# Kernel optimization log

Measured on AMD Instinct MI355X. Metric: run time of the kernel, lower is better.

The kernel has to match this reference:

```python
import jax, jax.numpy as jnp
import numpy as np

B, N, C, D = 4, 8192, 256, 256
WS = [2048, 4096, 8192]
RS = [1, 2, 4]
HEAD_IDX = 0


def setup_inputs() -> dict:
    key = jax.random.key(0)
    k1, k2, k3, k4 = jax.random.split(key, 4)
    scale = 1.0 / np.sqrt(C).astype(np.float32)
    x = jax.random.normal(k1, (B, N, C), jnp.float32)
    Wq = jax.random.normal(k2, (C, D), jnp.float32) * scale
    Wk = jax.random.normal(k3, (C, D), jnp.float32) * scale
    Wv = jax.random.normal(k4, (C, D), jnp.float32) * scale
    return {"x": x, "Wq": Wq, "Wk": Wk, "Wv": Wv}


def _causal_attn(v, Wq, Wk, Wv):
    # v: [Bseg, m, c] -> out [Bseg, m, D], denom [Bseg, m] (= sum_k exp(score))
    q = v @ Wq
    k = v @ Wk
    val = v @ Wv
    scores = jnp.einsum('bqd,bkd->bqk', q, k) / jnp.sqrt(jnp.asarray(D, v.dtype))
    m = v.shape[1]
    mask = jnp.tril(jnp.ones((m, m), bool))
    scores = jnp.where(mask, scores, -jnp.inf)
    mx = scores.max(-1)  # diagonal always unmasked -> finite
    e = jnp.exp(scores - mx[..., None])
    ssum = e.sum(-1)
    out = jnp.einsum('bqk,bkd->bqd', e, val) / ssum[..., None]
    denom = ssum * jnp.exp(mx)  # unnormalized softmax denominator
    return out, denom


def _dilated_forward(x, Wq, Wk, Wv):
    b, n, c = x.shape
    segs, idx_list = [], []
    for w, r in zip(WS, RS):
        off = HEAD_IDX % r
        s_cnt = n // w
        # [b, s, m, c] strided gather (offset::r within each window of size w)
        xr = x.reshape(b, s_cnt, w, c)[:, :, off::r, :]
        # segment-major then batch, matching torch.cat(..., dim=0) order
        segs.append(jnp.transpose(xr, (1, 0, 2, 3)).reshape(s_cnt * b, -1, c))
        pos = jnp.arange(off, w, r)
        idx_list.append(jnp.arange(s_cnt)[:, None] * w + pos[None, :])  # [s, m]
    batched = jnp.concatenate(segs, 0)  # [28, 2048, c]
    o_b, den_b = _causal_attn(batched, Wq, Wk, Wv)

    # per-token denominator sums across overlapping segments (scatter-add)
    sums = jnp.zeros((b, n), x.dtype)
    per_cfg = []
    start = 0
    for (w, r), idx in zip(zip(WS, RS), idx_list):
        s_cnt = n // w
        cnt = s_cnt * b
        o = jnp.transpose(o_b[start:start + cnt].reshape(s_cnt, b, -1, D), (1, 0, 2, 3))
        d = jnp.transpose(den_b[start:start + cnt].reshape(s_cnt, b, -1), (1, 0, 2))
        start += cnt
        flat_idx = idx.reshape(-1)  # [s*m]
        o_f = o.reshape(b, -1, D)
        d_f = d.reshape(b, -1)
        per_cfg.append((o_f, d_f, flat_idx))
        sums = sums.at[:, flat_idx].add(d_f)

    # weighted scatter-add of outputs, alpha = denom / denom_sum
    out = jnp.zeros((b, n, D), x.dtype)
    for o_f, d_f, flat_idx in per_cfg:
        alphas = d_f / sums[:, flat_idx]
        out = out.at[:, flat_idx, :].add(o_f * alphas[..., None])
    return out


def reference(x, Wq, Wk, Wv):
    return _dilated_forward(x, Wq, Wk, Wv)
```

## Files before the change

kernel.cpp:

```cpp
#include <hip/hip_runtime.h>
#include <hip/hip_bf16.h>

typedef __bf16 bf16;
typedef unsigned short u16;
typedef bf16 bf16x8 __attribute__((ext_vector_type(8)));
typedef bf16 bf16x2 __attribute__((ext_vector_type(2)));
typedef u16  u16x8  __attribute__((ext_vector_type(8)));
typedef u16  u16x4  __attribute__((ext_vector_type(4)));
typedef float f32x4 __attribute__((ext_vector_type(4)));
typedef float f32x16 __attribute__((ext_vector_type(16)));

#define MFMA16(a,b,c) __builtin_amdgcn_mfma_f32_16x16x32_bf16((a),(b),(c),0,0,0)
#define MFMA32(a,b,c) __builtin_amdgcn_mfma_f32_32x32x16_bf16((a),(b),(c),0,0,0)
#define QSCALE 0.09016844005625f

__device__ inline unsigned pack2(float a, float b) {
    bf16x2 t; t[0] = (bf16)a; t[1] = (bf16)b;
    return __builtin_bit_cast(unsigned, t);
}

__device__ __forceinline__ void load_lds16(const void* g, void* l) {
    __builtin_amdgcn_global_load_lds(
        (const __attribute__((address_space(1))) unsigned*)g,
        (__attribute__((address_space(3))) unsigned*)l, 16, 0, 0);
}

__device__ const unsigned short g_items[24] = {
    (unsigned short)(15 | (0u<<4) | (32u<<5)),
    (unsigned short)(14 | (0u<<4) | (32u<<5)),
    (unsigned short)(13 | (0u<<4) | (32u<<5)),
    (unsigned short)(12 | (0u<<4) | (32u<<5)),
    (unsigned short)(11 | (0u<<4) | (32u<<5)),
    (unsigned short)(10 | (0u<<4) | (32u<<5)),
    (unsigned short)( 9 | (0u<<4) | (32u<<5)),
    (unsigned short)( 8 | (0u<<4) | (32u<<5)),
    (unsigned short)(15 | (1u<<4) | (64u<<5)),
    (unsigned short)( 7 | (0u<<4) | (32u<<5)),
    (unsigned short)(14 | (1u<<4) | (60u<<5)),
    (unsigned short)( 6 | (0u<<4) | (28u<<5)),
    (unsigned short)(13 | (1u<<4) | (56u<<5)),
    (unsigned short)( 5 | (0u<<4) | (24u<<5)),
    (unsigned short)(12 | (1u<<4) | (52u<<5)),
    (unsigned short)( 4 | (0u<<4) | (20u<<5)),
    (unsigned short)(11 | (1u<<4) | (48u<<5)),
    (unsigned short)( 3 | (0u<<4) | (16u<<5)),
    (unsigned short)(10 | (1u<<4) | (44u<<5)),
    (unsigned short)( 2 | (0u<<4) | (12u<<5)),
    (unsigned short)( 9 | (1u<<4) | (40u<<5)),
    (unsigned short)( 1 | (0u<<4) | ( 8u<<5)),
    (unsigned short)( 8 | (1u<<4) | (36u<<5)),
    (unsigned short)( 0 | (0u<<4) | ( 4u<<5)),
};

__global__ void cvt_w(const float* __restrict__ Wq, const float* __restrict__ Wk,
                      const float* __restrict__ Wv, bf16* __restrict__ Wbt) {
    int idx = blockIdx.x * 256 + threadIdx.x;
    int which = idx >> 16;
    int rem = idx & 65535;
    int c = rem >> 8, d = rem & 255;
    const float* W = (which == 0) ? Wq : (which == 1) ? Wk : Wv;
    Wbt[(size_t)which * 65536 + d * 256 + c] = (bf16)W[c * 256 + d];
}

__global__ __launch_bounds__(256, 2)
void qkv_gemm(const float* __restrict__ x, const bf16* __restrict__ Wbt,
              bf16* __restrict__ Qb, bf16* __restrict__ Kb,
              bf16* __restrict__ Vtt1, bf16* __restrict__ Vtt2, bf16* __restrict__ Vtt4) {
    __shared__ __align__(16) u16 lA[2][64 * 136];
    __shared__ __align__(16) u16 lB[2][64 * 136];
    __shared__ __align__(16) u16 lT[64 * 72];
    int mt = blockIdx.x;
    int tid = threadIdx.x, wv = tid >> 6, lane = tid & 63;
    int l15 = lane & 15, quad = lane >> 4;

    const float* Ax = x + (size_t)(mt * 64) * 256;
    int row = tid >> 2, c0 = (tid & 3) * 32;

    #pragma unroll
    for (int kh = 0; kh < 2; kh++)
        #pragma unroll
        for (int i = 0; i < 4; i++) {
            float4 f0 = *(const float4*)(Ax + row * 256 + kh * 128 + c0 + i * 8);
            float4 f1 = *(const float4*)(Ax + row * 256 + kh * 128 + c0 + i * 8 + 4);
            bf16x8 v;
            v[0] = (bf16)f0.x; v[1] = (bf16)f0.y; v[2] = (bf16)f0.z; v[3] = (bf16)f0.w;
            v[4] = (bf16)f1.x; v[5] = (bf16)f1.y; v[6] = (bf16)f1.z; v[7] = (bf16)f1.w;
            *(bf16x8*)((bf16*)lA[kh] + row * 136 + c0 + i * 8) = v;
        }

    auto stageW = [&](const bf16* Bw, int t, int bs) {
        int kh = t >> 2, nt = t & 3;
        #pragma unroll
        for (int i = 0; i < 4; i++)
            *(bf16x8*)((bf16*)lB[bs] + row * 136 + c0 + i * 8) =
                *(const bf16x8*)(Bw + (size_t)(nt * 64 + row) * 256 + kh * 128 + c0 + i * 8);
    };

    for (int which = 0; which < 3; which++) {
        f32x4 acc[4][4] = {};
        const bf16* Bw = Wbt + (size_t)which * 65536;
        stageW(Bw, 0, 0);
        for (int t = 0; t < 8; t++) {
            __syncthreads();
            if (t + 1 < 8) stageW(Bw, t + 1, (t + 1) & 1);
            int kh = t >> 2, nt = t & 3;
            #pragma unroll
            for (int ks = 0; ks < 4; ks++) {
                bf16x8 a = *(const bf16x8*)((bf16*)lA[kh] + (wv * 16 + l15) * 136 + ks * 32 + quad * 8);
                #pragma unroll
                for (int ns = 0; ns < 4; ns++) {
                    bf16x8 b2 = *(const bf16x8*)((bf16*)lB[t & 1] + (ns * 16 + l15) * 136 + ks * 32 + quad * 8);
                    acc[nt][ns] = MFMA16(a, b2, acc[nt][ns]);
                }
            }
        }

        float sc = (which == 0) ? QSCALE : 1.0f;
        for (int nt = 0; nt < 4; nt++) {
            __syncthreads();
            if (which < 2) {
                #pragma unroll
                for (int ns = 0; ns < 4; ns++)
                    #pragma unroll
                    for (int r = 0; r < 4; r++) {
                        bf16 v = (bf16)(acc[nt][ns][r] * sc);
                        lT[(wv * 16 + quad * 4 + r) * 72 + ns * 16 + l15] = *(u16*)&v;
                    }
                __syncthreads();
                bf16* outp = (which == 0) ? Qb : Kb;
                int tokl = tid >> 2, ch = tid & 3;
                u16x8 v0 = *(u16x8*)(lT + tokl * 72 + ch * 16);
                u16x8 v1 = *(u16x8*)(lT + tokl * 72 + ch * 16 + 8);
                u16* dst = (u16*)outp + (size_t)(mt * 64 + tokl) * 256 + nt * 64 + ch * 16;
                *(u16x8*)dst = v0;
                *(u16x8*)(dst + 8) = v1;
            } else {
                #pragma unroll
                for (int ns = 0; ns < 4; ns++)
                    #pragma unroll
                    for (int r = 0; r < 4; r++) {
                        bf16 v = (bf16)acc[nt][ns][r];
                        lT[(ns * 16 + l15) * 72 + wv * 16 + quad * 4 + r] = *(u16*)&v;
                    }
                __syncthreads();
                int gtok = mt * 64;
                int bL = gtok >> 13, n0 = gtok & 8191;
                int d_l = tid >> 2, q = tid & 3;
                int dg = nt * 64 + d_l;
                {
                    int s1 = n0 >> 11, j1 = n0 & 2047;
                    u16* dst = (u16*)Vtt1 + ((size_t)(bL * 4 + s1) * 64 + (j1 >> 5) + (q >> 1)) * 8192
                               + (size_t)dg * 32 + (q & 1) * 16;
                    u16x8 a0 = *(u16x8*)(lT + d_l * 72 + q * 16);
                    u16x8 a1 = *(u16x8*)(lT + d_l * 72 + q * 16 + 8);
                    *(u16x8*)dst = a0; *(u16x8*)(dst + 8) = a1;
                }
                {
                    int s2 = n0 >> 12, j2 = (n0 & 4095) >> 1;
                    u16x8 e;
                    #pragma unroll
                    for (int i = 0; i < 8; i++) e[i] = lT[d_l * 72 + q * 16 + 2 * i];
                    u16* dst = (u16*)Vtt2 + ((size_t)(bL * 2 + s2) * 64 + (j2 >> 5)) * 8192
                               + (size_t)dg * 32 + q * 8;
                    *(u16x8*)dst = e;
                }
                {
                    int j4 = n0 >> 2;
                    u16x4 e;
                    #pragma unroll
                    for (int i = 0; i < 4; i++) e[i] = lT[d_l * 72 + q * 16 + 4 * i];
                    u16* dst = (u16*)Vtt4 + ((size_t)bL * 64 + (j4 >> 5)) * 8192
                               + (size_t)dg * 32 + (j4 & 31) + q * 4;
                    *(u16x4*)dst = e;
                }
            }
        }
    }
}

__global__ __launch_bounds__(256, 2)
void attn(const bf16* __restrict__ Qb, const bf16* __restrict__ Kb,
          const bf16* __restrict__ Vtt1, const bf16* __restrict__ Vtt2,
          const bf16* __restrict__ Vtt4,
          float* __restrict__ O1, float* __restrict__ O2, float* __restrict__ O4,
          float* __restrict__ D1, float* __restrict__ D2, float* __restrict__ D4,
          float* __restrict__ PO, float* __restrict__ PD) {
    __shared__ __align__(16) char K_l[2][16384];
    __shared__ __align__(16) char V_l[2][16384];

    const int tid = threadIdx.x, wv = tid >> 6, lane = tid & 63;
    const int l31 = lane & 31, hi = lane >> 5;

    const int item = (int)blockIdx.x;
    const unsigned e = g_items[item / 28];
    const int seg = item % 28;
    const int qt  = e & 15;
    const int ci  = (e >> 4) & 1;
    const int kt0 = ci << 5;
    const int kt1 = e >> 5;

    int lr, ss, b;
    if (seg < 16)      { lr = 0; ss = seg >> 2;        b = seg & 3;        }
    else if (seg < 24) { lr = 1; ss = (seg - 16) >> 2; b = (seg - 16) & 3; }
    else               { lr = 2; ss = 0;               b = seg - 24;       }
    const int rr = 1 << lr;
    const size_t base = (size_t)b * 8192 + (size_t)ss * (2048 << lr);
    const size_t pbase = (size_t)b * (8192 >> lr) + (size_t)ss * 2048;
    const int segi = (lr == 0) ? (b * 4 + ss) : (lr == 1) ? (b * 2 + ss) : b;
    const u16* Vseg = (const u16*)((lr == 0) ? Vtt1 : (lr == 1) ? Vtt2 : Vtt4)
                      + (size_t)segi * 524288;
    float* Op = (lr == 0) ? O1 : (lr == 1) ? O2 : O4;
    float* Dp = (lr == 0) ? D1 : (lr == 1) ? D2 : D4;

    const int ql = qt * 128 + wv * 32 + l31;
    const u16* Kp = (const u16*)Kb + base * 256;

    bf16x8 qf[16];
    {
        const bf16* qp = Qb + (base + (size_t)ql * rr) * 256 + hi * 8;
        #pragma unroll
        for (int ks = 0; ks < 16; ks++) qf[ks] = *(const bf16x8*)(qp + ks * 16);
    }

    auto stage = [&](int t, int bs) {
        #pragma unroll
        for (int i = 0; i < 4; i++) {
            const u16* src = Kp + (size_t)((t * 32 + (tid & 31)) * rr) * 256
                             + (i * 8 + (tid >> 5)) * 8;
            load_lds16(src, &K_l[bs][i * 4096 + wv * 1024]);
        }
        #pragma unroll
        for (int i = 0; i < 4; i++) {
            const u16* src = Vseg + (size_t)t * 8192 + (size_t)tid * 32 + i * 8;
            load_lds16(src, &V_l[bs][i * 4096 + wv * 1024]);
        }
    };

    f32x16 o[8] = {};
    float m_run = -1e30f, l_run = 0.f;

    stage(kt0, 0);

    const int dtile = 4 * qt + wv;
    for (int kt = kt0; kt < kt1; kt++) {
        const int buf = (kt - kt0) & 1;
        asm volatile("s_waitcnt vmcnt(0)" ::: "memory");
        __builtin_amdgcn_s_barrier();
        __builtin_amdgcn_sched_barrier(0);
        if (kt + 1 < kt1) stage(kt + 1, buf ^ 1);

        if (kt <= dtile) {
            const char* Kbl = K_l[buf];
            const char* Vbl = V_l[buf];

            f32x16 sv = {};
            __builtin_amdgcn_s_setprio(1);
            #pragma unroll
            for (int ks = 0; ks < 16; ks++) {
                bf16x8 kf = *(const bf16x8*)(Kbl + ks * 1024 + hi * 512 + l31 * 16);
                sv = MFMA32(kf, qf[ks], sv);
            }
            __builtin_amdgcn_s_setprio(0);

            float mx = -1e30f;
            const bool diag = (kt == dtile);
            #pragma unroll
            for (int r = 0; r < 16; r++) {
                float v = sv[r];
                if (diag) {
                    int key = kt * 32 + (r & 3) + 8 * (r >> 2) + 4 * hi;
                    if (key > ql) v = -1e30f;
                    sv[r] = v;
                }
                mx = fmaxf(mx, v);
            }
            mx = fmaxf(mx, __shfl_xor(mx, 32));

            if (__any(mx > m_run + 12.0f)) {
                float mnew = fmaxf(m_run, mx);
                float fac = exp2f(m_run - mnew);
                l_run *= fac;
                #pragma unroll
                for (int dg = 0; dg < 8; dg++)
                    #pragma unroll
                    for (int r = 0; r < 16; r++) o[dg][r] *= fac;
                m_run = mnew;
            }

            float rs = 0.f;
            #pragma unroll
            for (int r = 0; r < 16; r++) {
                float e2 = exp2f(sv[r] - m_run);
                sv[r] = e2;
                rs += e2;
            }
            rs += __shfl_xor(rs, 32);
            l_run += rs;

            unsigned pk[8];
            #pragma unroll
            for (int rq = 0; rq < 4; rq++) {
                pk[2 * rq]     = pack2(sv[4 * rq],     sv[4 * rq + 1]);
                pk[2 * rq + 1] = pack2(sv[4 * rq + 2], sv[4 * rq + 3]);
            }
            #pragma unroll
            for (int st = 0; st < 2; st++) {
                unsigned p0 = pk[4 * st],     p1 = pk[4 * st + 1];
                unsigned p2 = pk[4 * st + 2], p3 = pk[4 * st + 3];
                unsigned s0 = (unsigned)__shfl_xor((int)p0, 32);
                unsigned s1 = (unsigned)__shfl_xor((int)p1, 32);
                unsigned s2 = (unsigned)__shfl_xor((int)p2, 32);
                unsigned s3 = (unsigned)__shfl_xor((int)p3, 32);
                union { unsigned u[4]; bf16x8 v; } pb;
                pb.u[0] = hi ? s2 : p0;
                pb.u[1] = hi ? s3 : p1;
                pb.u[2] = hi ? p2 : s0;
                pb.u[3] = hi ? p3 : s1;
                __builtin_amdgcn_s_setprio(1);
                #pragma unroll
                for (int dg = 0; dg < 8; dg++) {
                    bf16x8 vf = *(const bf16x8*)(Vbl + (st * 2 + hi) * 4096 + dg * 512 + l31 * 16);
                    o[dg] = MFMA32(vf, pb.v, o[dg]);
                }
                __builtin_amdgcn_s_setprio(0);
            }
        }
    }

    float invl = 1.0f / l_run;
    size_t prow;
    float *obase, *dbase;
    if (ci == 0) { prow = pbase + (size_t)ql;                    obase = Op; dbase = Dp; }
    else         { prow = (size_t)seg * 1024 + (size_t)(ql - 1024); obase = PO; dbase = PD; }
    if (hi == 0) dbase[prow] = l_run * exp2f(m_run);
    float* orow = obase + prow * 256 + hi * 4;
    #pragma unroll
    for (int dg = 0; dg < 8; dg++)
        #pragma unroll
        for (int rq = 0; rq < 4; rq++) {
            f32x4 v;
            v[0] = o[dg][4 * rq]     * invl;
            v[1] = o[dg][4 * rq + 1] * invl;
            v[2] = o[dg][4 * rq + 2] * invl;
            v[3] = o[dg][4 * rq + 3] * invl;
            *(f32x4*)(orow + dg * 32 + rq * 8) = v;
        }
}

__global__ void finalize(float* __restrict__ out, const float* __restrict__ O2,
                         const float* __restrict__ O4,
                         const float* __restrict__ D1, const float* __restrict__ D2,
                         const float* __restrict__ D4,
                         const float* __restrict__ PO, const float* __restrict__ PD) {
    int g = blockIdx.x * 256 + threadIdx.x;
    int t = g >> 6, dc = (g & 63) * 4;
    int b = t >> 13, n = t & 8191;
    float d1 = D1[t];
    float4 o1 = *(float4*)(out + (size_t)t * 256 + dc);
    float ax = o1.x * d1, ay = o1.y * d1, az = o1.z * d1, aw = o1.w * d1;
    float den = d1;
    {
        int j1 = n & 2047;
        if (j1 >= 1024) {
            size_t pp = (size_t)(4 * (n >> 11) + b) * 1024 + (j1 - 1024);
            float dp = PD[pp];
            const float4 op = *(const float4*)(PO + pp * 256 + dc);
            ax += op.x * dp; ay += op.y * dp; az += op.z * dp; aw += op.w * dp;
            den += dp;
        }
    }
    if ((n & 1) == 0) {
        int s2 = n >> 12, j2 = (n & 4095) >> 1;
        int pos2 = b * 4096 + s2 * 2048 + j2;
        float d2 = D2[pos2];
        const float4 o2 = *(const float4*)(O2 + (size_t)pos2 * 256 + dc);
        ax += o2.x * d2; ay += o2.y * d2; az += o2.z * d2; aw += o2.w * d2;
        den += d2;
        if (j2 >= 1024) {
            size_t pp = (size_t)(16 + 4 * s2 + b) * 1024 + (j2 - 1024);
            float dp = PD[pp];
            const float4 op = *(const float4*)(PO + pp * 256 + dc);
            ax += op.x * dp; ay += op.y * dp; az += op.z * dp; aw += op.w * dp;
            den += dp;
        }
    }
    if ((n & 3) == 0) {
        int j4 = n >> 2;
        int pos4 = b * 2048 + j4;
        float d4 = D4[pos4];
        const float4 o4 = *(const float4*)(O4 + (size_t)pos4 * 256 + dc);
        ax += o4.x * d4; ay += o4.y * d4; az += o4.z * d4; aw += o4.w * d4;
        den += d4;
        if (j4 >= 1024) {
            size_t pp = (size_t)(24 + b) * 1024 + (j4 - 1024);
            float dp = PD[pp];
            const float4 op = *(const float4*)(PO + pp * 256 + dc);
            ax += op.x * dp; ay += op.y * dp; az += op.z * dp; aw += op.w * dp;
            den += dp;
        }
    }
    float inv = 1.0f / den;
    float4 r; r.x = ax * inv; r.y = ay * inv; r.z = az * inv; r.w = aw * inv;
    *(float4*)(out + (size_t)t * 256 + dc) = r;
}

extern "C" void kernel_launch(void* const* d_in, const int* in_sizes, int n_in,
                              void* d_out, int out_size, void* d_ws, size_t ws_size,
                              hipStream_t stream) {
    const float* x  = (const float*)d_in[0];
    const float* Wq = (const float*)d_in[1];
    const float* Wk = (const float*)d_in[2];
    const float* Wv = (const float*)d_in[3];
    float* out = (float*)d_out;

    char* ws = (char*)d_ws;
    bf16* Qb   = (bf16*)(ws);
    bf16* Kb   = (bf16*)(ws + 16777216);
    bf16* Vtt1 = (bf16*)(ws + 33554432);
    bf16* Vtt2 = (bf16*)(ws + 50331648);
    bf16* Vtt4 = (bf16*)(ws + 58720256);
    bf16* Wbt  = (bf16*)(ws + 62914560);
    float* O2  = (float*)(ws + 63307776);
    float* O4  = (float*)(ws + 80084992);
    float* D1  = (float*)(ws + 88473600);
    float* D2  = (float*)(ws + 88604672);
    float* D4  = (float*)(ws + 88670208);
    float* PO  = (float*)(ws + 88703232);
    float* PD  = (float*)(ws + 118063360);

    cvt_w<<<768, 256, 0, stream>>>(Wq, Wk, Wv, Wbt);
    qkv_gemm<<<512, 256, 0, stream>>>(x, Wbt, Qb, Kb, Vtt1, Vtt2, Vtt4);
    attn<<<672, 256, 0, stream>>>(Qb, Kb, Vtt1, Vtt2, Vtt4, out, O2, O4,
                                  D1, D2, D4, PO, PD);
    finalize<<<8192, 256, 0, stream>>>(out, O2, O4, D1, D2, D4, PO, PD);
}
```

Baseline: 236.7 us.

## Prefetch weight tiles into registers and batch QKV epilogue stores

The QKV GEMM now loads the next weight tile from global memory into registers before the MFMA loop and writes it to LDS afterwards, so the global load latency is hidden behind compute. The epilogue is restructured to stage all four output column tiles in a single LDS buffer that reuses the A/B shared memory, followed by one synchronisation and wide stores, instead of four sync-separated passes. The V scatter into the three dilated layouts is done from registers with per-thread contiguous stores. This adds register pressure, and only the QKV projection kernel is affected, not the attention kernel.

```diff
diff --git a/kernel.cpp b/kernel.cpp
--- a/kernel.cpp
+++ b/kernel.cpp
@@ -66,15 +66,18 @@
 void qkv_gemm(const float* __restrict__ x, const bf16* __restrict__ Wbt,
               bf16* __restrict__ Qb, bf16* __restrict__ Kb,
               bf16* __restrict__ Vtt1, bf16* __restrict__ Vtt2, bf16* __restrict__ Vtt4) {
-    __shared__ __align__(16) u16 lA[2][64 * 136];
-    __shared__ __align__(16) u16 lB[2][64 * 136];
-    __shared__ __align__(16) u16 lT[64 * 72];
+    __shared__ __align__(16) u16 lS[34816];
+    u16* lA = lS;
+    u16* lB = lS + 17408;
+
     int mt = blockIdx.x;
     int tid = threadIdx.x, wv = tid >> 6, lane = tid & 63;
     int l15 = lane & 15, quad = lane >> 4;
 
     const float* Ax = x + (size_t)(mt * 64) * 256;
     int row = tid >> 2, c0 = (tid & 3) * 32;
+    int gtok = mt * 64;
+    int bL = gtok >> 13, n0 = gtok & 8191;
 
     #pragma unroll
     for (int kh = 0; kh < 2; kh++)
@@ -85,96 +88,125 @@
             bf16x8 v;
             v[0] = (bf16)f0.x; v[1] = (bf16)f0.y; v[2] = (bf16)f0.z; v[3] = (bf16)f0.w;
             v[4] = (bf16)f1.x; v[5] = (bf16)f1.y; v[6] = (bf16)f1.z; v[7] = (bf16)f1.w;
-            *(bf16x8*)((bf16*)lA[kh] + row * 136 + c0 + i * 8) = v;
-        }
-
-    auto stageW = [&](const bf16* Bw, int t, int bs) {
-        int kh = t >> 2, nt = t & 3;
-        #pragma unroll
-        for (int i = 0; i < 4; i++)
-            *(bf16x8*)((bf16*)lB[bs] + row * 136 + c0 + i * 8) =
-                *(const bf16x8*)(Bw + (size_t)(nt * 64 + row) * 256 + kh * 128 + c0 + i * 8);
-    };
+            *(bf16x8*)((bf16*)lA + kh * 8704 + row * 136 + c0 + i * 8) = v;
+        }
 
     for (int which = 0; which < 3; which++) {
         f32x4 acc[4][4] = {};
         const bf16* Bw = Wbt + (size_t)which * 65536;
-        stageW(Bw, 0, 0);
+        bf16x8 wreg[4];
+
+        #pragma unroll
+        for (int i = 0; i < 4; i++)
+            wreg[i] = *(const bf16x8*)(Bw + (size_t)row * 256 + c0 + i * 8);
+        #pragma unroll
+        for (int i = 0; i < 4; i++)
+            *(bf16x8*)((bf16*)lB + row * 136 + c0 + i * 8) = wreg[i];
+
         for (int t = 0; t < 8; t++) {
             __syncthreads();
-            if (t + 1 < 8) stageW(Bw, t + 1, (t + 1) & 1);
+            if (t + 1 < 8) {
+                int kh2 = (t + 1) >> 2, nt2 = (t + 1) & 3;
+                #pragma unroll
+                for (int i = 0; i < 4; i++)
+                    wreg[i] = *(const bf16x8*)(Bw + (size_t)(nt2 * 64 + row) * 256
+                                               + kh2 * 128 + c0 + i * 8);
+            }
             int kh = t >> 2, nt = t & 3;
             #pragma unroll
             for (int ks = 0; ks < 4; ks++) {
-                bf16x8 a = *(const bf16x8*)((bf16*)lA[kh] + (wv * 16 + l15) * 136 + ks * 32 + quad * 8);
+                bf16x8 a = *(const bf16x8*)((bf16*)lA + kh * 8704 + (wv * 16 + l15) * 136
+                                            + ks * 32 + quad * 8);
                 #pragma unroll
                 for (int ns = 0; ns < 4; ns++) {
-                    bf16x8 b2 = *(const bf16x8*)((bf16*)lB[t & 1] + (ns * 16 + l15) * 136 + ks * 32 + quad * 8);
+                    bf16x8 b2 = *(const bf16x8*)((bf16*)lB + (t & 1) * 8704
+                                                 + (ns * 16 + l15) * 136 + ks * 32 + quad * 8);
                     acc[nt][ns] = MFMA16(a, b2, acc[nt][ns]);
                 }
             }
-        }
-
-        float sc = (which == 0) ? QSCALE : 1.0f;
-        for (int nt = 0; nt < 4; nt++) {
-            __syncthreads();
-            if (which < 2) {
+            if (t + 1 < 8) {
+                #pragma unroll
+                for (int i = 0; i < 4; i++)
+                    *(bf16x8*)((bf16*)lB + ((t + 1) & 1) * 8704 + row * 136 + c0 + i * 8) = wreg[i];
+            }
+        }
+        __syncthreads();
+
+        if (which < 2) {
+            u16* lT = lB;
+            float sc = (which == 0) ? QSCALE : 1.0f;
+            #pragma unroll
+            for (int nt = 0; nt < 4; nt++)
                 #pragma unroll
                 for (int ns = 0; ns < 4; ns++)
                     #pragma unroll
                     for (int r = 0; r < 4; r++) {
                         bf16 v = (bf16)(acc[nt][ns][r] * sc);
-                        lT[(wv * 16 + quad * 4 + r) * 72 + ns * 16 + l15] = *(u16*)&v;
+                        lT[(wv * 16 + quad * 4 + r) * 264 + nt * 64 + ns * 16 + l15] = *(u16*)&v;
                     }
-                __syncthreads();
-                bf16* outp = (which == 0) ? Qb : Kb;
-                int tokl = tid >> 2, ch = tid & 3;
-                u16x8 v0 = *(u16x8*)(lT + tokl * 72 + ch * 16);
-                u16x8 v1 = *(u16x8*)(lT + tokl * 72 + ch * 16 + 8);
-                u16* dst = (u16*)outp + (size_t)(mt * 64 + tokl) * 256 + nt * 64 + ch * 16;
-                *(u16x8*)dst = v0;
-                *(u16x8*)(dst + 8) = v1;
-            } else {
+            __syncthreads();
+            bf16* outp = (which == 0) ? Qb : Kb;
+            int tokl = tid >> 2, ch = tid & 3;
+            u16* dst = (u16*)outp + (size_t)(gtok + tokl) * 256 + ch * 64;
+            const u16* srcp = lT + tokl * 264 + ch * 64;
+            #pragma unroll
+            for (int i = 0; i < 8; i++)
+                *(u16x8*)(dst + i * 8) = *(const u16x8*)(srcp + i * 8);
+        } else {
+            u16* lT = lS;
+            #pragma unroll
+            for (int nt = 0; nt < 4; nt++)
                 #pragma unroll
                 for (int ns = 0; ns < 4; ns++)
                     #pragma unroll
                     for (int r = 0; r < 4; r++) {
                         bf16 v = (bf16)acc[nt][ns][r];
-                        lT[(ns * 16 + l15) * 72 + wv * 16 + quad * 4 + r] = *(u16*)&v;
+                        lT[(nt * 64 + ns * 16 + l15) * 72 + wv * 16 + quad * 4 + r] = *(u16*)&v;
                     }
-                __syncthreads();
-                int gtok = mt * 64;
-                int bL = gtok >> 13, n0 = gtok & 8191;
-                int d_l = tid >> 2, q = tid & 3;
-                int dg = nt * 64 + d_l;
-                {
-                    int s1 = n0 >> 11, j1 = n0 & 2047;
-                    u16* dst = (u16*)Vtt1 + ((size_t)(bL * 4 + s1) * 64 + (j1 >> 5) + (q >> 1)) * 8192
-                               + (size_t)dg * 32 + (q & 1) * 16;
-                    u16x8 a0 = *(u16x8*)(lT + d_l * 72 + q * 16);
-                    u16x8 a1 = *(u16x8*)(lT + d_l * 72 + q * 16 + 8);
-                    *(u16x8*)dst = a0; *(u16x8*)(dst + 8) = a1;
+            __syncthreads();
+            int dg = tid;
+            u16x8 v[8];
+            #pragma unroll
+            for (int i = 0; i < 8; i++) v[i] = *(const u16x8*)(lT + dg * 72 + i * 8);
+            {
+                int s1 = n0 >> 11, j1 = n0 & 2047;
+                u16* d0 = (u16*)Vtt1 + (size_t)((bL * 4 + s1) * 64 + (j1 >> 5)) * 8192
+                          + (size_t)dg * 32;
+                u16* d1 = d0 + 8192;
+                *(u16x8*)(d0)      = v[0]; *(u16x8*)(d0 + 8)  = v[1];
+                *(u16x8*)(d0 + 16) = v[2]; *(u16x8*)(d0 + 24) = v[3];
+                *(u16x8*)(d1)      = v[4]; *(u16x8*)(d1 + 8)  = v[5];
+                *(u16x8*)(d1 + 16) = v[6]; *(u16x8*)(d1 + 24) = v[7];
+            }
+            {
+                int s2 = n0 >> 12, j2 = (n0 & 4095) >> 1;
+                u16x8 e0, e1, e2, e3;
+                #pragma unroll
+                for (int j = 0; j < 4; j++) {
+                    e0[j] = v[0][2 * j]; e0[4 + j] = v[1][2 * j];
+                    e1[j] = v[2][2 * j]; e1[4 + j] = v[3][2 * j];
+                    e2[j] = v[4][2 * j]; e2[4 + j] = v[5][2 * j];
+                    e3[j] = v[6][2 * j]; e3[4 + j] = v[7][2 * j];
                 }
-                {
-                    int s2 = n0 >> 12, j2 = (n0 & 4095) >> 1;
-                    u16x8 e;
-                    #pragma unroll
-                    for (int i = 0; i < 8; i++) e[i] = lT[d_l * 72 + q * 16 + 2 * i];
-                    u16* dst = (u16*)Vtt2 + ((size_t)(bL * 2 + s2) * 64 + (j2 >> 5)) * 8192
-                               + (size_t)dg * 32 + q * 8;
-                    *(u16x8*)dst = e;
+                u16* d = (u16*)Vtt2 + (size_t)((bL * 2 + s2) * 64 + (j2 >> 5)) * 8192
+                         + (size_t)dg * 32;
+                *(u16x8*)(d)      = e0; *(u16x8*)(d + 8)  = e1;
+                *(u16x8*)(d + 16) = e2; *(u16x8*)(d + 24) = e3;
+            }
+            {
+                int j4 = n0 >> 2;
+                u16x8 f0, f1;
+                #pragma unroll
+                for (int j = 0; j < 4; j++) {
+                    f0[2 * j]     = v[j][0];     f0[2 * j + 1] = v[j][4];
+                    f1[2 * j]     = v[4 + j][0]; f1[2 * j + 1] = v[4 + j][4];
                 }
-                {
-                    int j4 = n0 >> 2;
-                    u16x4 e;
-                    #pragma unroll
-                    for (int i = 0; i < 4; i++) e[i] = lT[d_l * 72 + q * 16 + 4 * i];
-                    u16* dst = (u16*)Vtt4 + ((size_t)bL * 64 + (j4 >> 5)) * 8192
-                               + (size_t)dg * 32 + (j4 & 31) + q * 4;
-                    *(u16x4*)dst = e;
-                }
-            }
-        }
+                u16* d = (u16*)Vtt4 + (size_t)(bL * 64 + (j4 >> 5)) * 8192
+                         + (size_t)dg * 32 + (j4 & 31);
+                *(u16x8*)(d) = f0; *(u16x8*)(d + 8) = f1;
+            }
+        }
+        __syncthreads();
     }
 }
 
```

Result: slower. 245.4 us (+3.6%).
